# Kernel optimization log

Measured on AMD Instinct MI355X. Metric: run time of the kernel, lower is better.

Reference implementation:

```python
import jax, jax.numpy as jnp
import numpy as np

D_MODEL = 1024
N_HEADS = 16
D_HEAD = D_MODEL // N_HEADS
QLEN = 512
MLEN = 512
BATCH = 8


def setup_inputs() -> dict:
    key = jax.random.key(0)
    ks = jax.random.split(key, 12)
    s = 0.02
    inputs = jax.random.normal(ks[0], (QLEN, BATCH, D_MODEL), jnp.float32)
    r = jax.random.normal(ks[1], (QLEN + MLEN, 1, D_MODEL), jnp.float32)
    u = jax.random.normal(ks[2], (N_HEADS, D_HEAD), jnp.float32) * s
    v = jax.random.normal(ks[3], (N_HEADS, D_HEAD), jnp.float32) * s
    mem = jax.random.normal(ks[4], (MLEN, BATCH, D_MODEL), jnp.float32)
    # attention params (Transformer-XL style): fused qkv, r-projection, output proj
    W_qkv = jax.random.normal(ks[5], (D_MODEL, 3 * D_MODEL), jnp.float32) * s
    W_r = jax.random.normal(ks[6], (D_MODEL, D_MODEL), jnp.float32) * s
    W_o = jax.random.normal(ks[7], (D_MODEL, D_MODEL), jnp.float32) * s
    # GRU params: input-hidden and hidden-hidden for gates (r, z, n), torch layout
    W_ih = jax.random.normal(ks[8], (3 * D_MODEL, D_MODEL), jnp.float32) * s
    W_hh = jax.random.normal(ks[9], (3 * D_MODEL, D_MODEL), jnp.float32) * s
    b_ih = jax.random.normal(ks[10], (3 * D_MODEL,), jnp.float32) * s
    b_hh = jax.random.normal(ks[11], (3 * D_MODEL,), jnp.float32) * s
    h0 = jnp.zeros((BATCH, D_MODEL), jnp.float32)
    return dict(inputs=inputs, r=r, u=u, v=v, mem=mem, W_qkv=W_qkv, W_r=W_r,
                W_o=W_o, W_ih=W_ih, W_hh=W_hh, b_ih=b_ih, b_hh=b_hh, h0=h0)


def _rel_shift(x):
    # x: [q, k, b, h] -> Transformer-XL relative shift
    q, k, b, h = x.shape
    zero_pad = jnp.zeros((q, 1, b, h), x.dtype)
    x_padded = jnp.concatenate([zero_pad, x], axis=1)        # [q, k+1, b, h]
    x_padded = x_padded.reshape(k + 1, q, b, h)
    return x_padded[1:].reshape(q, k, b, h)


def _attention(inputs, r, u, v, mem, W_qkv, W_r, W_o):
    qlen, bsz, _ = inputs.shape
    cat = jnp.concatenate([mem, inputs], axis=0)             # [klen, b, d]
    klen = cat.shape[0]
    qkv = cat @ W_qkv                                        # [klen, b, 3d]
    w_head_q, w_head_k, w_head_v = jnp.split(qkv, 3, axis=-1)
    w_head_q = w_head_q[-qlen:]                              # [q, b, d]
    r_head_k = (r[:, 0, :] @ W_r).reshape(klen, N_HEADS, D_HEAD)  # [k, h, dh]

    q_ = w_head_q.reshape(qlen, bsz, N_HEADS, D_HEAD)
    k_ = w_head_k.reshape(klen, bsz, N_HEADS, D_HEAD)
    v_ = w_head_v.reshape(klen, bsz, N_HEADS, D_HEAD)

    AC = jnp.einsum('ibhd,jbhd->ijbh', q_ + u[None, None], k_)
    BD = jnp.einsum('ibhd,jhd->ijbh', q_ + v[None, None], r_head_k)
    BD = _rel_shift(BD)
    scale = 1.0 / np.sqrt(D_HEAD)
    attn_score = (AC + BD) * scale                           # [q, k, b, h]

    # causal mask with memory: query i attends to keys j <= i + mlen
    mlen = klen - qlen
    i = jnp.arange(qlen)[:, None]
    j = jnp.arange(klen)[None, :]
    mask = j > (i + mlen)                                    # [q, k]
    attn_score = jnp.where(mask[:, :, None, None], -jnp.inf, attn_score)

    attn_prob = jax.nn.softmax(attn_score, axis=1)
    attn_vec = jnp.einsum('ijbh,jbhd->ibhd', attn_prob, v_)
    attn_vec = attn_vec.reshape(qlen, bsz, D_MODEL)
    return attn_vec @ W_o                                    # [q, b, d]


def _gru(x, h0, W_ih, W_hh, b_ih, b_hh):
    # x: [T, B, D]; torch GRU cell math
    Wi_r, Wi_z, Wi_n = jnp.split(W_ih, 3, axis=0)
    Wh_r, Wh_z, Wh_n = jnp.split(W_hh, 3, axis=0)
    bi_r, bi_z, bi_n = jnp.split(b_ih, 3)
    bh_r, bh_z, bh_n = jnp.split(b_hh, 3)

    # precompute input projections for all timesteps
    xr = x @ Wi_r.T + bi_r
    xz = x @ Wi_z.T + bi_z
    xn = x @ Wi_n.T + bi_n

    def step(h, xs):
        xr_t, xz_t, xn_t = xs
        r = jax.nn.sigmoid(xr_t + h @ Wh_r.T + bh_r)
        z = jax.nn.sigmoid(xz_t + h @ Wh_z.T + bh_z)
        n = jnp.tanh(xn_t + r * (h @ Wh_n.T + bh_n))
        h_new = (1.0 - z) * n + z * h
        return h_new, h_new

    _, ys = jax.lax.scan(step, h0, (xr, xz, xn))
    return ys                                                # [T, B, D]


def reference(inputs, r, u, v, mem, W_qkv, W_r, W_o, W_ih, W_hh, b_ih, b_hh, h0):
    y = _attention(inputs, r, u, v, mem, W_qkv, W_r, W_o)
    return _gru(y, h0, W_ih, W_hh, b_ih, b_hh)
```

## Files before the change

### kernel.cpp

```cpp
#include <hip/hip_runtime.h>
#include <math.h>


typedef short bf16x8 __attribute__((ext_vector_type(8)));
typedef float f32x4 __attribute__((ext_vector_type(4)));

union FragU { uint4 u; bf16x8 h; };

#define APAD 65

__device__ inline void split2(float x0, float x1, unsigned& hi, unsigned& lo) {
    unsigned u0 = __float_as_uint(x0), u1 = __float_as_uint(x1);
    float h0 = __uint_as_float(u0 & 0xffff0000u);
    float h1 = __uint_as_float(u1 & 0xffff0000u);
    unsigned l0 = __float_as_uint(x0 - h0), l1 = __float_as_uint(x1 - h1);
    hi = (u0 >> 16) | (u1 & 0xffff0000u);
    lo = (l0 >> 16) | (l1 & 0xffff0000u);
}

__device__ __forceinline__ unsigned long long ld_coh64(const void* p) {
    return __hip_atomic_load((const unsigned long long*)p, __ATOMIC_RELAXED,
                             __HIP_MEMORY_SCOPE_AGENT);
}
__device__ __forceinline__ void st_coh64(void* p, unsigned long long v) {
    __hip_atomic_store((unsigned long long*)p, v, __ATOMIC_RELAXED,
                       __HIP_MEMORY_SCOPE_AGENT);
}

__device__ __forceinline__ void gl_lds16(const uint4* g, uint4* l) {
    __builtin_amdgcn_global_load_lds(
        (const __attribute__((address_space(1))) uint4*)g,
        (__attribute__((address_space(3))) uint4*)l, 16, 0, 0);
}

__device__ __forceinline__ void split_store8(
    const float* x, unsigned* out, int n, int K, int kt, int j)
{
    unsigned h[4], l[4];
    split2(x[0], x[1], h[0], l[0]);
    split2(x[2], x[3], h[1], l[1]);
    split2(x[4], x[5], h[2], l[2]);
    split2(x[6], x[7], h[3], l[3]);
    unsigned* base = out + (size_t)n * K + kt * 32;
    *(uint4*)(base + (((2 * j) ^ (n & 7)) * 4))     = make_uint4(h[0], h[1], h[2], h[3]);
    *(uint4*)(base + (((2 * j + 1) ^ (n & 7)) * 4)) = make_uint4(l[0], l[1], l[2], l[3]);
}

#define SEG0 1048576
#define SEG1 1441792
#define SEG2 1572864
#define SEG3 1703936
#define SEG4 2097152
#define SEG5 2228224

__global__ __launch_bounds__(256) void prep_all(
    const float* __restrict__ mem, const float* __restrict__ inputs,
    const float* __restrict__ Wqkv, const float* __restrict__ Wr,
    const float* __restrict__ Wo, const float* __restrict__ Wih,
    const float* __restrict__ r_in,
    unsigned* __restrict__ catP, unsigned* __restrict__ WqkvP,
    unsigned* __restrict__ WrP, unsigned* __restrict__ WoP,
    unsigned* __restrict__ WihP, unsigned* __restrict__ rP)
{
    int idx = blockIdx.x * 256 + threadIdx.x;
    if (idx >= SEG5) return;
    float x[8];
    if (idx < SEG0) {
        int c = idx & 127, n = idx >> 7;
        int kt = c >> 2, j = c & 3, k = kt * 32 + j * 8;
        const float* src = (n < 4096) ? (mem + (size_t)n * 1024 + k)
                                      : (inputs + (size_t)(n - 4096) * 1024 + k);
        float4 a = *(const float4*)src, b = *(const float4*)(src + 4);
        x[0]=a.x; x[1]=a.y; x[2]=a.z; x[3]=a.w; x[4]=b.x; x[5]=b.y; x[6]=b.z; x[7]=b.w;
        split_store8(x, catP, n, 1024, kt, j);
    } else if (idx < SEG3) {
        int i, Nr, ldw; const float* W; unsigned* out;
        if (idx < SEG1)      { i = idx - SEG0; Nr = 3072; ldw = 3072; W = Wqkv; out = WqkvP; }
        else if (idx < SEG2) { i = idx - SEG1; Nr = 1024; ldw = 1024; W = Wr;   out = WrP;  }
        else                 { i = idx - SEG2; Nr = 1024; ldw = 1024; W = Wo;   out = WoP;  }
        int n = i % Nr, c = i / Nr;
        int kt = c >> 2, j = c & 3, k = kt * 32 + j * 8;
        #pragma unroll
        for (int q = 0; q < 8; ++q) x[q] = W[(size_t)(k + q) * ldw + n];
        split_store8(x, out, n, 1024, kt, j);
    } else {
        int i; const float* W; unsigned* out;
        if (idx < SEG4) { i = idx - SEG3; W = Wih;  out = WihP; }
        else            { i = idx - SEG4; W = r_in; out = rP;   }
        int c = i & 127, n = i >> 7;
        int kt = c >> 2, j = c & 3, k = kt * 32 + j * 8;
        float4 a = *(const float4*)(W + (size_t)n * 1024 + k);
        float4 b = *(const float4*)(W + (size_t)n * 1024 + k + 4);
        x[0]=a.x; x[1]=a.y; x[2]=a.z; x[3]=a.w; x[4]=b.x; x[5]=b.y; x[6]=b.z; x[7]=b.w;
        split_store8(x, out, n, 1024, kt, j);
    }
}

template<bool BIAS, bool SPLITOUT>
__global__ __launch_bounds__(256) void gemm_pp(
    const uint4* __restrict__ Ap4, const uint4* __restrict__ Bp4,
    const float* __restrict__ bias, float* __restrict__ C,
    unsigned* __restrict__ Cp, int K, int ldc)
{
    __shared__ uint4 SH[2048];
    uint4* Ab = SH;
    uint4* Bb = SH + 1024;
    int tid = threadIdx.x;
    int lane = tid & 63, wid = tid >> 6;
    int wr = wid >> 1, wc = wid & 1;
    int n0 = blockIdx.x * 128, m0 = blockIdx.y * 128;
    int r15 = lane & 15, s = lane >> 4;
    int r4 = (lane >> 4) * 4;
    int K4 = K >> 2;

    f32x4 acc[4][4];
    #pragma unroll
    for (int i = 0; i < 4; ++i)
        #pragma unroll
        for (int j = 0; j < 4; ++j) acc[i][j] = 0.0f;

    for (int kt = 0; kt < (K >> 5); ++kt) {
        #pragma unroll
        for (int q = 0; q < 4; ++q) {
            int base = q * 256 + wid * 64;
            int idx  = base + lane;
            int row = idx >> 3, slot = idx & 7;
            gl_lds16(Ap4 + (size_t)(m0 + row) * K4 + kt * 8 + slot, &Ab[base]);
            gl_lds16(Bp4 + (size_t)(n0 + row) * K4 + kt * 8 + slot, &Bb[base]);
        }
        __syncthreads();
        FragU ahi[4], alo[4], bhi[4], blo[4];
        #pragma unroll
        for (int f = 0; f < 4; ++f) {
            int ar = wr * 64 + f * 16 + r15;
            ahi[f].u = Ab[ar * 8 + ((2 * s) ^ (ar & 7))];
            alo[f].u = Ab[ar * 8 + ((2 * s + 1) ^ (ar & 7))];
            int br = wc * 64 + f * 16 + r15;
            bhi[f].u = Bb[br * 8 + ((2 * s) ^ (br & 7))];
            blo[f].u = Bb[br * 8 + ((2 * s + 1) ^ (br & 7))];
        }
        #pragma unroll
        for (int fi = 0; fi < 4; ++fi)
            #pragma unroll
            for (int fj = 0; fj < 4; ++fj) {
                acc[fi][fj] = __builtin_amdgcn_mfma_f32_16x16x32_bf16(ahi[fi].h, bhi[fj].h, acc[fi][fj], 0, 0, 0);
                acc[fi][fj] = __builtin_amdgcn_mfma_f32_16x16x32_bf16(ahi[fi].h, blo[fj].h, acc[fi][fj], 0, 0, 0);
                acc[fi][fj] = __builtin_amdgcn_mfma_f32_16x16x32_bf16(alo[fi].h, bhi[fj].h, acc[fi][fj], 0, 0, 0);
            }
        __syncthreads();
    }

    if (!SPLITOUT) {
        #pragma unroll
        for (int fj = 0; fj < 4; ++fj) {
            int n = n0 + wc * 64 + fj * 16 + r15;
            float bv = BIAS ? bias[n] : 0.f;
            #pragma unroll
            for (int fi = 0; fi < 4; ++fi) {
                int m = m0 + wr * 64 + fi * 16 + r4;
                #pragma unroll
                for (int r = 0; r < 4; ++r)
                    C[(size_t)(m + r) * ldc + n] = acc[fi][fj][r] + bv;
            }
        }
    } else {
        float* Cs = (float*)SH;
        #pragma unroll
        for (int half = 0; half < 2; ++half) {
            __syncthreads();
            if (wr == half) {
                #pragma unroll
                for (int fi = 0; fi < 4; ++fi)
                    #pragma unroll
                    for (int fj = 0; fj < 4; ++fj)
                        #pragma unroll
                        for (int r = 0; r < 4; ++r)
                            Cs[(fi * 16 + r4 + r) * 128 + wc * 64 + fj * 16 + r15] = acc[fi][fj][r];
            }
            __syncthreads();
            #pragma unroll
            for (int q = 0; q < 4; ++q) {
                int oc = q * 256 + tid;
                int lr = oc >> 4, oct = oc & 15;
                float x[8];
                *(float4*)&x[0] = *(float4*)&Cs[lr * 128 + oct * 8];
                *(float4*)&x[4] = *(float4*)&Cs[lr * 128 + oct * 8 + 4];
                int m = m0 + half * 64 + lr;
                int k = n0 + oct * 8;
                split_store8(x, Cp, m, ldc, k >> 5, (k >> 3) & 3);
            }
        }
    }
}

__global__ __launch_bounds__(256) void attn_fused(
    const float* __restrict__ qkv, const float* __restrict__ rk,
    const float* __restrict__ u_, const float* __restrict__ v_,
    unsigned* __restrict__ y1P)
{
    __shared__ float qu[64][APAD], qv[64][APAD], Kt[64][APAD], Vt[64][APAD];
    __shared__ float RKs[128][APAD];
    __shared__ float S[64][APAD];

    int tid = threadIdx.x;
    int it = blockIdx.x, b = blockIdx.y, h = blockIdx.z;
    int i0 = it * 64;
    int ti = tid >> 4, tj = tid & 15;

    {
        int r = tid >> 2, c0 = (tid & 3) * 16;
        size_t base = ((size_t)(i0 + r + 512) * 8 + b) * 3072 + h * 64;
        #pragma unroll
        for (int q = 0; q < 4; ++q) {
            int c = c0 + q * 4;
            float4 qq = *(const float4*)&qkv[base + c];
            float4 uu = *(const float4*)&u_[h * 64 + c];
            float4 vv = *(const float4*)&v_[h * 64 + c];
            *(float4*)&qu[r][c] = make_float4(qq.x + uu.x, qq.y + uu.y, qq.z + uu.z, qq.w + uu.w);
            *(float4*)&qv[r][c] = make_float4(qq.x + vv.x, qq.y + vv.y, qq.z + vv.z, qq.w + vv.w);
        }
    }

    float m[4] = {-1e30f, -1e30f, -1e30f, -1e30f};
    float l[4] = {0.f, 0.f, 0.f, 0.f};
    float Od[4][4] = {};
    int njt = it + 9;

    for (int jt = 0; jt < njt; ++jt) {
        int j0 = jt * 64;
        __syncthreads();
        {
            int r = tid >> 2, c0 = (tid & 3) * 16;
            size_t kb = ((size_t)(j0 + r) * 8 + b) * 3072 + 1024 + h * 64;
            #pragma unroll
            for (int q = 0; q < 4; ++q) {
                int c = c0 + q * 4;
                *(float4*)&Kt[r][c] = *(const float4*)&qkv[kb + c];
                *(float4*)&Vt[r][c] = *(const float4*)&qkv[kb + 1024 + c];
            }
        }
        {
            int r2 = tid >> 1, c0 = (tid & 1) * 32;
            int jj = j0 - i0 + 448 + r2;
            jj = jj < 0 ? 0 : (jj > 1023 ? 1023 : jj);
            size_t rb = (size_t)jj * 1024 + h * 64;
            #pragma unroll
            for (int q = 0; q < 8; ++q) {
                int c = c0 + q * 4;
                *(float4*)&RKs[r2][c] = *(const float4*)&rk[rb + c];
            }
        }
        __syncthreads();

        float acc[4][4] = {};
        int jlb = (tj - ti) * 4 + 60;
        #pragma unroll 4
        for (int d4 = 0; d4 < 64; d4 += 4) {
            float4 Aq[4], Cq[4], Kv[4], Rv[7];
            #pragma unroll
            for (int i = 0; i < 4; ++i) {
                Aq[i] = *(float4*)&qu[ti * 4 + i][d4];
                Cq[i] = *(float4*)&qv[ti * 4 + i][d4];
                Kv[i] = *(float4*)&Kt[tj * 4 + i][d4];
            }
            #pragma unroll
            for (int t = 0; t < 7; ++t)
                Rv[t] = *(float4*)&RKs[jlb + t][d4];
            #pragma unroll
            for (int i = 0; i < 4; ++i)
                #pragma unroll
                for (int j = 0; j < 4; ++j) {
                    float4 kk = Kv[j];
                    float4 rr = Rv[j - i + 3];
                    acc[i][j] += Aq[i].x * kk.x + Aq[i].y * kk.y + Aq[i].z * kk.z + Aq[i].w * kk.w
                               + Cq[i].x * rr.x + Cq[i].y * rr.y + Cq[i].z * rr.z + Cq[i].w * rr.w;
                }
        }
        #pragma unroll
        for (int i = 0; i < 4; ++i) {
            int gi = i0 + ti * 4 + i;
            float mx = -1e30f;
            #pragma unroll
            for (int j = 0; j < 4; ++j) {
                int gj = j0 + tj * 4 + j;
                float vS = acc[i][j] * 0.125f;
                if (gj > gi + 512) vS = -1e30f;
                acc[i][j] = vS;
                mx = fmaxf(mx, vS);
            }
            mx = fmaxf(mx, __shfl_xor(mx, 1));
            mx = fmaxf(mx, __shfl_xor(mx, 2));
            mx = fmaxf(mx, __shfl_xor(mx, 4));
            mx = fmaxf(mx, __shfl_xor(mx, 8));
            float mn = fmaxf(m[i], mx);
            float sc = __expf(m[i] - mn);
            m[i] = mn;
            float4 pv;
            pv.x = __expf(acc[i][0] - mn);
            pv.y = __expf(acc[i][1] - mn);
            pv.z = __expf(acc[i][2] - mn);
            pv.w = __expf(acc[i][3] - mn);
            *(float4*)&S[ti * 4 + i][tj * 4] = pv;
            float ps = pv.x + pv.y + pv.z + pv.w;
            ps += __shfl_xor(ps, 1);
            ps += __shfl_xor(ps, 2);
            ps += __shfl_xor(ps, 4);
            ps += __shfl_xor(ps, 8);
            l[i] = l[i] * sc + ps;
            #pragma unroll
            for (int j2 = 0; j2 < 4; ++j2) Od[i][j2] *= sc;
        }
        asm volatile("" ::: "memory");
        #pragma unroll 4
        for (int jb = 0; jb < 64; jb += 4) {
            float4 p0 = *(float4*)&S[ti * 4 + 0][jb];
            float4 p1 = *(float4*)&S[ti * 4 + 1][jb];
            float4 p2 = *(float4*)&S[ti * 4 + 2][jb];
            float4 p3 = *(float4*)&S[ti * 4 + 3][jb];
            float4 v0 = *(float4*)&Vt[jb + 0][tj * 4];
            float4 v1 = *(float4*)&Vt[jb + 1][tj * 4];
            float4 v2 = *(float4*)&Vt[jb + 2][tj * 4];
            float4 v3 = *(float4*)&Vt[jb + 3][tj * 4];
            float4 pr[4] = {p0, p1, p2, p3};
            #pragma unroll
            for (int i = 0; i < 4; ++i) {
                Od[i][0] += pr[i].x * v0.x + pr[i].y * v1.x + pr[i].z * v2.x + pr[i].w * v3.x;
                Od[i][1] += pr[i].x * v0.y + pr[i].y * v1.y + pr[i].z * v2.y + pr[i].w * v3.y;
                Od[i][2] += pr[i].x * v0.z + pr[i].y * v1.z + pr[i].z * v2.z + pr[i].w * v3.z;
                Od[i][3] += pr[i].x * v0.w + pr[i].y * v1.w + pr[i].z * v2.w + pr[i].w * v3.w;
            }
        }
    }
    #pragma unroll
    for (int i = 0; i < 4; ++i) {
        int ri = ti * 4 + i;
        float inv = 1.f / l[i];
        float4 o = make_float4(Od[i][0] * inv, Od[i][1] * inv, Od[i][2] * inv, Od[i][3] * inv);
        int n = (i0 + ri) * 8 + b;
        unsigned hw0, hw1, lw0, lw1;
        split2(o.x, o.y, hw0, lw0);
        split2(o.z, o.w, hw1, lw1);
        int kt2 = 2 * h + (tj >> 3);
        int j2 = (tj >> 1) & 3;
        int wo = (tj & 1) * 2;
        unsigned* bp = y1P + (size_t)n * 1024 + kt2 * 32;
        *(uint2*)(bp + (((2 * j2)     ^ (n & 7)) * 4) + wo) = make_uint2(hw0, hw1);
        *(uint2*)(bp + (((2 * j2 + 1) ^ (n & 7)) * 4) + wo) = make_uint2(lw0, lw1);
    }
}

__global__ __launch_bounds__(256) void prep_whh(
    const float* __restrict__ Whh, uint4* __restrict__ outp)
{
    int idx = blockIdx.x * 256 + threadIdx.x;
    if (idx >= 393216) return;
    int lane = idx & 63;
    int rest = idx >> 6;
    int gate = rest % 3;
    int kt   = (rest / 3) & 31;
    int g64  = rest / 96;
    int n = gate * 1024 + g64 * 16 + (lane & 15);
    int k = kt * 32 + (lane >> 4) * 8;
    const float* src = Whh + (size_t)n * 1024 + k;
    float4 x0 = *(const float4*)src, x1 = *(const float4*)(src + 4);
    unsigned h[4], l[4];
    split2(x0.x, x0.y, h[0], l[0]);
    split2(x0.z, x0.w, h[1], l[1]);
    split2(x1.x, x1.y, h[2], l[2]);
    split2(x1.z, x1.w, h[3], l[3]);
    outp[((size_t)rest * 2 + 0) * 64 + lane] = make_uint4(h[0], h[1], h[2], h[3]);
    outp[((size_t)rest * 2 + 1) * 64 + lane] = make_uint4(l[0], l[1], l[2], l[3]);
}

__global__ __launch_bounds__(256, 1) void gru_persist2(
    const float* __restrict__ h0, float* __restrict__ hA, float* __restrict__ hB,
    const uint4* __restrict__ WhhG, const float* __restrict__ bhh,
    const float* __restrict__ xg, float* __restrict__ out,
    unsigned* __restrict__ flags)
{
    __shared__ uint4 Bf[4096];
    __shared__ float red[3][64][4];
    int tid = threadIdx.x;
    int lane = tid & 63, wv = tid >> 6;
    int g64 = blockIdx.x;

    int col = lane & 15;
    int d0 = g64 * 16 + (lane >> 4) * 4;
    bool act = (wv == 0) && (col < 8);
    float4 br4 = make_float4(0, 0, 0, 0), bz4 = br4, bn4 = br4;
    if (act) {
        br4 = *(const float4*)&bhh[d0];
        bz4 = *(const float4*)&bhh[1024 + d0];
        bn4 = *(const float4*)&bhh[2048 + d0];
    }
    const uint4* wb = WhhG + (size_t)g64 * 12288 + (wv < 3 ? wv : 0) * 128 + lane;

    for (int t = 0; t < 512; ++t) {
        const float* hi_ = (t == 0) ? h0 : ((t & 1) ? hA : hB);
        float* ho = (t & 1) ? hB : hA;

        float4 xr4, xz4, xn4;
        unsigned long long hp01 = 0, hp23 = 0;
        if (act) {
            size_t xb = ((size_t)t * 8 + col) * 3072 + d0;
            xr4 = *(const float4*)&xg[xb];
            xz4 = *(const float4*)&xg[xb + 1024];
            xn4 = *(const float4*)&xg[xb + 2048];
            hp01 = ld_coh64(hi_ + col * 1024 + d0);
            hp23 = ld_coh64(hi_ + col * 1024 + d0 + 2);
        }

        uint4 wA[16], wB[16];
        #pragma unroll
        for (int q = 0; q < 8; ++q) {
            wA[2 * q]     = wb[q * 384];
            wA[2 * q + 1] = wb[q * 384 + 64];
        }

        unsigned long long hq[16];
        #pragma unroll
        for (int i = 0; i < 4; ++i) {
            int s = i * 256 + tid;
            const float* hp = hi_ + (s & 7) * 1024 + (s >> 5) * 32 + ((s >> 3) & 3) * 8;
            #pragma unroll
            for (int q = 0; q < 4; ++q) hq[i * 4 + q] = ld_coh64(hp + q * 2);
        }
        #pragma unroll
        for (int i = 0; i < 4; ++i) {
            int s = i * 256 + tid;
            int b = s & 7, oct = (s >> 3) & 3, kt = s >> 5;
            float x[8];
            #pragma unroll
            for (int q = 0; q < 4; ++q) {
                x[2 * q]     = __uint_as_float((unsigned)(hq[i * 4 + q] & 0xffffffffu));
                x[2 * q + 1] = __uint_as_float((unsigned)(hq[i * 4 + q] >> 32));
            }
            unsigned hh[4], ll[4];
            split2(x[0], x[1], hh[0], ll[0]);
            split2(x[2], x[3], hh[1], ll[1]);
            split2(x[4], x[5], hh[2], ll[2]);
            split2(x[6], x[7], hh[3], ll[3]);
            int ln = oct * 16 + b;
            Bf[(kt * 2 + 0) * 64 + ln] = make_uint4(hh[0], hh[1], hh[2], hh[3]);
            Bf[(kt * 2 + 1) * 64 + ln] = make_uint4(ll[0], ll[1], ll[2], ll[3]);
        }
        __syncthreads();

        f32x4 acc = 0.0f;
        #define GRU_LOAD(dst, c0)                                   \
            _Pragma("unroll")                                       \
            for (int q = 0; q < 8; ++q) {                           \
                dst[2 * q]     = wb[((c0) * 8 + q) * 384];          \
                dst[2 * q + 1] = wb[((c0) * 8 + q) * 384 + 64];     \
            }
        #define GRU_COMP(src, c0)                                   \
            _Pragma("unroll")                                       \
            for (int q = 0; q < 8; ++q) {                           \
                int kt = (c0) * 8 + q;                              \
                FragU ah, al, bh, bl;                               \
                ah.u = src[2 * q]; al.u = src[2 * q + 1];           \
                bh.u = Bf[(kt * 2 + 0) * 64 + lane];                \
                bl.u = Bf[(kt * 2 + 1) * 64 + lane];                \
                acc = __builtin_amdgcn_mfma_f32_16x16x32_bf16(ah.h, bh.h, acc, 0, 0, 0); \
                acc = __builtin_amdgcn_mfma_f32_16x16x32_bf16(ah.h, bl.h, acc, 0, 0, 0); \
                acc = __builtin_amdgcn_mfma_f32_16x16x32_bf16(al.h, bh.h, acc, 0, 0, 0); \
            }
        if (wv < 3) {
            GRU_LOAD(wB, 1);
            GRU_COMP(wA, 0);
            GRU_LOAD(wA, 2);
            GRU_COMP(wB, 1);
            GRU_LOAD(wB, 3);
            GRU_COMP(wA, 2);
            GRU_COMP(wB, 3);
            *(f32x4*)&red[wv][lane][0] = acc;
        }
        #undef GRU_LOAD
        #undef GRU_COMP
        __syncthreads();

        if (act) {
            f32x4 aR = *(f32x4*)&red[0][lane][0];
            f32x4 aZ = *(f32x4*)&red[1][lane][0];
            f32x4 aN = *(f32x4*)&red[2][lane][0];
            float xr[4] = {xr4.x, xr4.y, xr4.z, xr4.w};
            float xz[4] = {xz4.x, xz4.y, xz4.z, xz4.w};
            float xn[4] = {xn4.x, xn4.y, xn4.z, xn4.w};
            float hp[4] = {__uint_as_float((unsigned)(hp01 & 0xffffffffu)),
                           __uint_as_float((unsigned)(hp01 >> 32)),
                           __uint_as_float((unsigned)(hp23 & 0xffffffffu)),
                           __uint_as_float((unsigned)(hp23 >> 32))};
            float br[4] = {br4.x, br4.y, br4.z, br4.w};
            float bz[4] = {bz4.x, bz4.y, bz4.z, bz4.w};
            float bn[4] = {bn4.x, bn4.y, bn4.z, bn4.w};
            float hn[4];
            #pragma unroll
            for (int r = 0; r < 4; ++r) {
                float rr = 1.f / (1.f + __expf(-(xr[r] + aR[r] + br[r])));
                float zz = 1.f / (1.f + __expf(-(xz[r] + aZ[r] + bz[r])));
                float nn = tanhf(xn[r] + rr * (aN[r] + bn[r]));
                hn[r] = (1.f - zz) * nn + zz * hp[r];
            }
            unsigned long long v01 = (unsigned long long)__float_as_uint(hn[0])
                                   | ((unsigned long long)__float_as_uint(hn[1]) << 32);
            unsigned long long v23 = (unsigned long long)__float_as_uint(hn[2])
                                   | ((unsigned long long)__float_as_uint(hn[3]) << 32);
            st_coh64(ho + col * 1024 + d0, v01);
            st_coh64(ho + col * 1024 + d0 + 2, v23);
            *(float4*)&out[((size_t)t * 8 + col) * 1024 + d0] =
                make_float4(hn[0], hn[1], hn[2], hn[3]);
        }

        if (t != 511) {
            __syncthreads();
            unsigned tgt = (unsigned)t + 1u;
            if (tid < 64) {
                if (tid == 0)
                    __hip_atomic_store(&flags[(size_t)g64 * 16], tgt,
                                       __ATOMIC_RELAXED, __HIP_MEMORY_SCOPE_AGENT);
                const unsigned* fp = &flags[(size_t)tid * 16];
                for (;;) {
                    unsigned f = __hip_atomic_load(fp, __ATOMIC_RELAXED,
                                                   __HIP_MEMORY_SCOPE_AGENT);
                    if (__all(f >= tgt)) break;
                }
            }
            __syncthreads();
        }
    }
}

__global__ __launch_bounds__(192, 1) void gru_step_mfma(
    const float* __restrict__ hin, float* __restrict__ hout,
    const uint4* __restrict__ WhhG, const float* __restrict__ bhh,
    const float* __restrict__ xg, float* __restrict__ out, int t)
{
    __shared__ uint4 Bf[4096];
    __shared__ float red[3][64][4];
    int tid = threadIdx.x;
    int lane = tid & 63, wv = tid >> 6;
    int g64 = blockIdx.x;

    int col = lane & 15;
    int d0 = g64 * 16 + (lane >> 4) * 4;
    bool act = (wv == 0) && (col < 8);
    float4 xr4, xz4, xn4, hp4, br4, bz4, bn4;
    if (act) {
        size_t xb = ((size_t)t * 8 + col) * 3072 + d0;
        xr4 = *(const float4*)&xg[xb];
        xz4 = *(const float4*)&xg[xb + 1024];
        xn4 = *(const float4*)&xg[xb + 2048];
        hp4 = *(const float4*)&hin[col * 1024 + d0];
        br4 = *(const float4*)&bhh[d0];
        bz4 = *(const float4*)&bhh[1024 + d0];
        bn4 = *(const float4*)&bhh[2048 + d0];
    }

    const uint4* wb = WhhG + (size_t)g64 * 12288 + wv * 128 + lane;
    uint4 wA[16], wB[16];
    #pragma unroll
    for (int q = 0; q < 8; ++q) {
        wA[2 * q]     = wb[q * 384];
        wA[2 * q + 1] = wb[q * 384 + 64];
    }

    for (int s = tid; s < 1024; s += 192) {
        int b = s & 7, oct = (s >> 3) & 3, kt = s >> 5;
        const float* hp = hin + b * 1024 + kt * 32 + oct * 8;
        float4 x0 = *(const float4*)hp, x1 = *(const float4*)(hp + 4);
        unsigned hh[4], ll[4];
        split2(x0.x, x0.y, hh[0], ll[0]);
        split2(x0.z, x0.w, hh[1], ll[1]);
        split2(x1.x, x1.y, hh[2], ll[2]);
        split2(x1.z, x1.w, hh[3], ll[3]);
        int ln = oct * 16 + b;
        Bf[(kt * 2 + 0) * 64 + ln] = make_uint4(hh[0], hh[1], hh[2], hh[3]);
        Bf[(kt * 2 + 1) * 64 + ln] = make_uint4(ll[0], ll[1], ll[2], ll[3]);
    }
    __syncthreads();

    f32x4 acc = 0.0f;
    #define GRU_LOAD(dst, c0)                                   \
        _Pragma("unroll")                                       \
        for (int q = 0; q < 8; ++q) {                           \
            dst[2 * q]     = wb[((c0) * 8 + q) * 384];          \
            dst[2 * q + 1] = wb[((c0) * 8 + q) * 384 + 64];     \
        }
    #define GRU_COMP(src, c0)                                   \
        _Pragma("unroll")                                       \
        for (int q = 0; q < 8; ++q) {                           \
            int kt = (c0) * 8 + q;                              \
            FragU ah, al, bh, bl;                               \
            ah.u = src[2 * q]; al.u = src[2 * q + 1];           \
            bh.u = Bf[(kt * 2 + 0) * 64 + lane];                \
            bl.u = Bf[(kt * 2 + 1) * 64 + lane];                \
            acc = __builtin_amdgcn_mfma_f32_16x16x32_bf16(ah.h, bh.h, acc, 0, 0, 0); \
            acc = __builtin_amdgcn_mfma_f32_16x16x32_bf16(ah.h, bl.h, acc, 0, 0, 0); \
            acc = __builtin_amdgcn_mfma_f32_16x16x32_bf16(al.h, bh.h, acc, 0, 0, 0); \
        }
    GRU_LOAD(wB, 1);
    GRU_COMP(wA, 0);
    GRU_LOAD(wA, 2);
    GRU_COMP(wB, 1);
    GRU_LOAD(wB, 3);
    GRU_COMP(wA, 2);
    GRU_COMP(wB, 3);
    #undef GRU_LOAD
    #undef GRU_COMP

    *(f32x4*)&red[wv][lane][0] = acc;
    __syncthreads();

    if (act) {
        f32x4 aR = *(f32x4*)&red[0][lane][0];
        f32x4 aZ = *(f32x4*)&red[1][lane][0];
        f32x4 aN = *(f32x4*)&red[2][lane][0];
        float xr[4] = {xr4.x, xr4.y, xr4.z, xr4.w};
        float xz[4] = {xz4.x, xz4.y, xz4.z, xz4.w};
        float xn[4] = {xn4.x, xn4.y, xn4.z, xn4.w};
        float hp[4] = {hp4.x, hp4.y, hp4.z, hp4.w};
        float br[4] = {br4.x, br4.y, br4.z, br4.w};
        float bz[4] = {bz4.x, bz4.y, bz4.z, bz4.w};
        float bn[4] = {bn4.x, bn4.y, bn4.z, bn4.w};
        float hn[4];
        #pragma unroll
        for (int r = 0; r < 4; ++r) {
            float rr = 1.f / (1.f + __expf(-(xr[r] + aR[r] + br[r])));
            float zz = 1.f / (1.f + __expf(-(xz[r] + aZ[r] + bz[r])));
            float nn = tanhf(xn[r] + rr * (aN[r] + bn[r]));
            hn[r] = (1.f - zz) * nn + zz * hp[r];
        }
        float4 hv = make_float4(hn[0], hn[1], hn[2], hn[3]);
        *(float4*)&hout[col * 1024 + d0] = hv;
        *(float4*)&out[((size_t)t * 8 + col) * 1024 + d0] = hv;
    }
}

extern "C" void kernel_launch(void* const* d_in, const int* in_sizes, int n_in,
                              void* d_out, int out_size, void* d_ws, size_t ws_size,
                              hipStream_t stream) {
    (void)in_sizes; (void)n_in; (void)out_size; (void)ws_size;
    const float* inputs = (const float*)d_in[0];
    const float* r_in   = (const float*)d_in[1];
    const float* u_in   = (const float*)d_in[2];
    const float* v_in   = (const float*)d_in[3];
    const float* mem    = (const float*)d_in[4];
    const float* Wqkv   = (const float*)d_in[5];
    const float* Wr     = (const float*)d_in[6];
    const float* Wo     = (const float*)d_in[7];
    const float* Wih    = (const float*)d_in[8];
    const float* Whh    = (const float*)d_in[9];
    const float* bih    = (const float*)d_in[10];
    const float* bhh    = (const float*)d_in[11];
    const float* h0     = (const float*)d_in[12];
    float* out = (float*)d_out;
    float* ws = (float*)d_ws;

    float*    qkv   = ws;
    float*    rk    = ws + 25165824;
    unsigned* y1P   = (unsigned*)(ws + 26214400);
    unsigned* y2P   = (unsigned*)(ws + 30408704);
    float*    xg    = ws + 34603008;
    float*    hA    = ws + 47185920;
    float*    hB    = ws + 47194112;
    unsigned* WqkvP = (unsigned*)(ws + 47202304);
    unsigned* WrP   = (unsigned*)(ws + 50348032);
    unsigned* WoP   = (unsigned*)(ws + 51396608);
    unsigned* WihP  = (unsigned*)(ws + 52445184);
    unsigned* flags = (unsigned*)(ws + 55590912);
    uint4*    WhhG  = (uint4*)qkv;
    unsigned* catP  = (unsigned*)xg;
    unsigned* rP    = (unsigned*)xg + 8388608;

    dim3 blk(256);
    hipMemsetAsync(flags, 0, 4096, stream);
    prep_all<<<8704, blk, 0, stream>>>(mem, inputs, Wqkv, Wr, Wo, Wih, r_in,
                                       catP, WqkvP, WrP, WoP, WihP, rP);

    gemm_pp<false, false><<<dim3(16, 32), blk, 0, stream>>>(
        (const uint4*)catP, (const uint4*)WqkvP + 1024 * 256, nullptr,
        qkv + 1024, nullptr, 1024, 3072);
    gemm_pp<false, false><<<dim3(24, 32), blk, 0, stream>>>(
        (const uint4*)catP + 4096 * 256, (const uint4*)WqkvP, nullptr,
        qkv + (size_t)4096 * 3072, nullptr, 1024, 3072);
    gemm_pp<false, false><<<dim3(8, 8), blk, 0, stream>>>(
        (const uint4*)rP, (const uint4*)WrP, nullptr, rk, nullptr, 1024, 1024);
    attn_fused<<<dim3(8, 8, 16), blk, 0, stream>>>(qkv, rk, u_in, v_in, y1P);
    prep_whh<<<1536, blk, 0, stream>>>(Whh, WhhG);
    gemm_pp<false, true><<<dim3(8, 32), blk, 0, stream>>>(
        (const uint4*)y1P, (const uint4*)WoP, nullptr, nullptr, y2P, 1024, 1024);
    gemm_pp<true, false><<<dim3(24, 32), blk, 0, stream>>>(
        (const uint4*)y2P, (const uint4*)WihP, bih, xg, nullptr, 1024, 3072);

    {
        const float* a0 = h0; float* a1 = hA; float* a2 = hB;
        const uint4* a3 = WhhG; const float* a4 = bhh; const float* a5 = xg;
        float* a6 = out; unsigned* a7 = flags;
        void* args[8] = {&a0, &a1, &a2, &a3, &a4, &a5, &a6, &a7};
        hipError_t e = hipLaunchCooperativeKernel((void*)gru_persist2,
                                                  dim3(64), dim3(256), args, 0, stream);
        if (e != hipSuccess) {
            const float* hin = h0;
            for (int s = 0; s < 512; ++s) {
                float* hp = (s & 1) ? hB : hA;
                gru_step_mfma<<<64, dim3(192), 0, stream>>>(hin, hp, WhhG, bhh, xg, out, s);
                hin = hp;
            }
        }
    }
}
```

Baseline: 4.735 ms.

## Overlap GRU input-projection GEMM with persistent recurrence in one cooperative kernel

Removes the separate xg GEMM launch and folds it into the cooperative GRU kernel. Extra blocks (64 beyond the 64 recurrence blocks) compute 128x128 tiles of the input projection and publish per-row-block completion counters. The recurrence blocks spin on those counters every 16 timesteps before reading xg with coherent loads. This overlaps the input-projection GEMM with the serial recurrence, at the cost of scalar atomic stores and spin-waiting. It also changes APAD from 65 to 68.

```diff
diff --git a/kernel.cpp b/kernel.cpp
--- a/kernel.cpp
+++ b/kernel.cpp
@@ -7,7 +7,9 @@
 
 union FragU { uint4 u; bf16x8 h; };
 
-#define APAD 65
+#define APAD 68
+#define ULO(v) __uint_as_float((unsigned)((v) & 0xffffffffu))
+#define UHI(v) __uint_as_float((unsigned)((v) >> 32))
 
 __device__ inline void split2(float x0, float x1, unsigned& hi, unsigned& lo) {
     unsigned u0 = __float_as_uint(x0), u1 = __float_as_uint(x1);
@@ -25,6 +27,9 @@
 __device__ __forceinline__ void st_coh64(void* p, unsigned long long v) {
     __hip_atomic_store((unsigned long long*)p, v, __ATOMIC_RELAXED,
                        __HIP_MEMORY_SCOPE_AGENT);
+}
+__device__ __forceinline__ void st_coh32(float* p, float v) {
+    __hip_atomic_store(p, v, __ATOMIC_RELAXED, __HIP_MEMORY_SCOPE_AGENT);
 }
 
 __device__ __forceinline__ void gl_lds16(const uint4* g, uint4* l) {
@@ -372,15 +377,84 @@
     outp[((size_t)rest * 2 + 1) * 64 + lane] = make_uint4(l[0], l[1], l[2], l[3]);
 }
 
-__global__ __launch_bounds__(256, 1) void gru_persist2(
+__global__ __launch_bounds__(256, 1) void gru_xg_fused(
     const float* __restrict__ h0, float* __restrict__ hA, float* __restrict__ hB,
     const uint4* __restrict__ WhhG, const float* __restrict__ bhh,
-    const float* __restrict__ xg, float* __restrict__ out,
-    unsigned* __restrict__ flags)
+    float* __restrict__ xg,
+    const uint4* __restrict__ y2P, const uint4* __restrict__ WihP,
+    const float* __restrict__ bih,
+    float* __restrict__ out, unsigned* __restrict__ flags,
+    unsigned* __restrict__ xgcnt)
 {
-    __shared__ uint4 Bf[4096];
-    __shared__ float red[3][64][4];
+    __shared__ uint4 SMEM[4288];
     int tid = threadIdx.x;
+
+    if (blockIdx.x >= 64) {
+        uint4* Ab = SMEM;
+        uint4* Bb = SMEM + 1024;
+        int lane = tid & 63, wid = tid >> 6;
+        int wr = wid >> 1, wc = wid & 1;
+        int r15 = lane & 15, s = lane >> 4;
+        int r4q = (lane >> 4) * 4;
+        for (int T = (int)blockIdx.x - 64; T < 768; T += 64) {
+            int m0 = (T / 24) * 128, n0 = (T % 24) * 128;
+            f32x4 acc[4][4];
+            #pragma unroll
+            for (int i = 0; i < 4; ++i)
+                #pragma unroll
+                for (int j = 0; j < 4; ++j) acc[i][j] = 0.0f;
+            for (int kt = 0; kt < 32; ++kt) {
+                #pragma unroll
+                for (int q = 0; q < 4; ++q) {
+                    int base = q * 256 + wid * 64;
+                    int idx  = base + lane;
+                    int row = idx >> 3, slot = idx & 7;
+                    gl_lds16(y2P + (size_t)(m0 + row) * 256 + kt * 8 + slot, &Ab[base]);
+                    gl_lds16(WihP + (size_t)(n0 + row) * 256 + kt * 8 + slot, &Bb[base]);
+                }
+                __syncthreads();
+                FragU ahi[4], alo[4], bhi[4], blo[4];
+                #pragma unroll
+                for (int f = 0; f < 4; ++f) {
+                    int ar = wr * 64 + f * 16 + r15;
+                    ahi[f].u = Ab[ar * 8 + ((2 * s) ^ (ar & 7))];
+                    alo[f].u = Ab[ar * 8 + ((2 * s + 1) ^ (ar & 7))];
+                    int br = wc * 64 + f * 16 + r15;
+                    bhi[f].u = Bb[br * 8 + ((2 * s) ^ (br & 7))];
+                    blo[f].u = Bb[br * 8 + ((2 * s + 1) ^ (br & 7))];
+                }
+                #pragma unroll
+                for (int fi = 0; fi < 4; ++fi)
+                    #pragma unroll
+                    for (int fj = 0; fj < 4; ++fj) {
+                        acc[fi][fj] = __builtin_amdgcn_mfma_f32_16x16x32_bf16(ahi[fi].h, bhi[fj].h, acc[fi][fj], 0, 0, 0);
+                        acc[fi][fj] = __builtin_amdgcn_mfma_f32_16x16x32_bf16(ahi[fi].h, blo[fj].h, acc[fi][fj], 0, 0, 0);
+                        acc[fi][fj] = __builtin_amdgcn_mfma_f32_16x16x32_bf16(alo[fi].h, bhi[fj].h, acc[fi][fj], 0, 0, 0);
+                    }
+                __syncthreads();
+            }
+            #pragma unroll
+            for (int fj = 0; fj < 4; ++fj) {
+                int n = n0 + wc * 64 + fj * 16 + r15;
+                float bv = bih[n];
+                #pragma unroll
+                for (int fi = 0; fi < 4; ++fi) {
+                    int mr = m0 + wr * 64 + fi * 16 + r4q;
+                    #pragma unroll
+                    for (int r = 0; r < 4; ++r)
+                        st_coh32(&xg[(size_t)(mr + r) * 3072 + n], acc[fi][fj][r] + bv);
+                }
+            }
+            __syncthreads();
+            if (tid == 0)
+                __hip_atomic_fetch_add(&xgcnt[(size_t)(T / 24) * 16], 1u,
+                                       __ATOMIC_RELAXED, __HIP_MEMORY_SCOPE_AGENT);
+        }
+        return;
+    }
+
+    uint4* Bf = SMEM;
+    float* red = (float*)(SMEM + 4096);
     int lane = tid & 63, wv = tid >> 6;
     int g64 = blockIdx.x;
 
@@ -399,13 +473,18 @@
         const float* hi_ = (t == 0) ? h0 : ((t & 1) ? hA : hB);
         float* ho = (t & 1) ? hB : hA;
 
-        float4 xr4, xz4, xn4;
+        unsigned long long xr01 = 0, xr23 = 0, xz01 = 0, xz23 = 0, xn01 = 0, xn23 = 0;
         unsigned long long hp01 = 0, hp23 = 0;
         if (act) {
+            if ((t & 15) == 0) {
+                const unsigned* xf = xgcnt + (size_t)(t >> 4) * 16;
+                while (__hip_atomic_load(xf, __ATOMIC_RELAXED,
+                                         __HIP_MEMORY_SCOPE_AGENT) < 24u) {}
+            }
             size_t xb = ((size_t)t * 8 + col) * 3072 + d0;
-            xr4 = *(const float4*)&xg[xb];
-            xz4 = *(const float4*)&xg[xb + 1024];
-            xn4 = *(const float4*)&xg[xb + 2048];
+            xr01 = ld_coh64(&xg[xb]);        xr23 = ld_coh64(&xg[xb + 2]);
+            xz01 = ld_coh64(&xg[xb + 1024]); xz23 = ld_coh64(&xg[xb + 1026]);
+            xn01 = ld_coh64(&xg[xb + 2048]); xn23 = ld_coh64(&xg[xb + 2050]);
             hp01 = ld_coh64(hi_ + col * 1024 + d0);
             hp23 = ld_coh64(hi_ + col * 1024 + d0 + 2);
         }
@@ -432,8 +511,8 @@
             float x[8];
             #pragma unroll
             for (int q = 0; q < 4; ++q) {
-                x[2 * q]     = __uint_as_float((unsigned)(hq[i * 4 + q] & 0xffffffffu));
-                x[2 * q + 1] = __uint_as_float((unsigned)(hq[i * 4 + q] >> 32));
+                x[2 * q]     = ULO(hq[i * 4 + q]);
+                x[2 * q + 1] = UHI(hq[i * 4 + q]);
             }
             unsigned hh[4], ll[4];
             split2(x[0], x[1], hh[0], ll[0]);
@@ -473,23 +552,20 @@
             GRU_LOAD(wB, 3);
             GRU_COMP(wA, 2);
             GRU_COMP(wB, 3);
-            *(f32x4*)&red[wv][lane][0] = acc;
+            *(f32x4*)&red[(wv * 64 + lane) * 4] = acc;
         }
         #undef GRU_LOAD
         #undef GRU_COMP
         __syncthreads();
 
         if (act) {
-            f32x4 aR = *(f32x4*)&red[0][lane][0];
-            f32x4 aZ = *(f32x4*)&red[1][lane][0];
-            f32x4 aN = *(f32x4*)&red[2][lane][0];
-            float xr[4] = {xr4.x, xr4.y, xr4.z, xr4.w};
-            float xz[4] = {xz4.x, xz4.y, xz4.z, xz4.w};
-            float xn[4] = {xn4.x, xn4.y, xn4.z, xn4.w};
-            float hp[4] = {__uint_as_float((unsigned)(hp01 & 0xffffffffu)),
-                           __uint_as_float((unsigned)(hp01 >> 32)),
-                           __uint_as_float((unsigned)(hp23 & 0xffffffffu)),
-                           __uint_as_float((unsigned)(hp23 >> 32))};
+            f32x4 aR = *(f32x4*)&red[(0 * 64 + lane) * 4];
+            f32x4 aZ = *(f32x4*)&red[(1 * 64 + lane) * 4];
+            f32x4 aN = *(f32x4*)&red[(2 * 64 + lane) * 4];
+            float xr[4] = {ULO(xr01), UHI(xr01), ULO(xr23), UHI(xr23)};
+            float xz[4] = {ULO(xz01), UHI(xz01), ULO(xz23), UHI(xz23)};
+            float xn[4] = {ULO(xn01), UHI(xn01), ULO(xn23), UHI(xn23)};
+            float hp[4] = {ULO(hp01), UHI(hp01), ULO(hp23), UHI(hp23)};
             float br[4] = {br4.x, br4.y, br4.z, br4.w};
             float bz[4] = {bz4.x, bz4.y, bz4.z, bz4.w};
             float bn[4] = {bn4.x, bn4.y, bn4.z, bn4.w};
@@ -668,12 +744,13 @@
     unsigned* WoP   = (unsigned*)(ws + 51396608);
     unsigned* WihP  = (unsigned*)(ws + 52445184);
     unsigned* flags = (unsigned*)(ws + 55590912);
+    unsigned* xgcnt = (unsigned*)(ws + 55590912) + 1024;
     uint4*    WhhG  = (uint4*)qkv;
     unsigned* catP  = (unsigned*)xg;
     unsigned* rP    = (unsigned*)xg + 8388608;
 
     dim3 blk(256);
-    hipMemsetAsync(flags, 0, 4096, stream);
+    (void)hipMemsetAsync(flags, 0, 6144, stream);
     prep_all<<<8704, blk, 0, stream>>>(mem, inputs, Wqkv, Wr, Wo, Wih, r_in,
                                        catP, WqkvP, WrP, WoP, WihP, rP);
 
@@ -689,17 +766,19 @@
     prep_whh<<<1536, blk, 0, stream>>>(Whh, WhhG);
     gemm_pp<false, true><<<dim3(8, 32), blk, 0, stream>>>(
         (const uint4*)y1P, (const uint4*)WoP, nullptr, nullptr, y2P, 1024, 1024);
-    gemm_pp<true, false><<<dim3(24, 32), blk, 0, stream>>>(
-        (const uint4*)y2P, (const uint4*)WihP, bih, xg, nullptr, 1024, 3072);
 
     {
         const float* a0 = h0; float* a1 = hA; float* a2 = hB;
-        const uint4* a3 = WhhG; const float* a4 = bhh; const float* a5 = xg;
-        float* a6 = out; unsigned* a7 = flags;
-        void* args[8] = {&a0, &a1, &a2, &a3, &a4, &a5, &a6, &a7};
-        hipError_t e = hipLaunchCooperativeKernel((void*)gru_persist2,
-                                                  dim3(64), dim3(256), args, 0, stream);
+        const uint4* a3 = WhhG; const float* a4 = bhh; float* a5 = xg;
+        const uint4* a6 = (const uint4*)y2P; const uint4* a7 = (const uint4*)WihP;
+        const float* a8 = bih; float* a9 = out;
+        unsigned* a10 = flags; unsigned* a11 = xgcnt;
+        void* args[12] = {&a0, &a1, &a2, &a3, &a4, &a5, &a6, &a7, &a8, &a9, &a10, &a11};
+        hipError_t e = hipLaunchCooperativeKernel((void*)gru_xg_fused,
+                                                  dim3(128), dim3(256), args, 0, stream);
         if (e != hipSuccess) {
+            gemm_pp<true, false><<<dim3(24, 32), blk, 0, stream>>>(
+                (const uint4*)y2P, (const uint4*)WihP, bih, xg, nullptr, 1024, 3072);
             const float* hin = h0;
             for (int s = 0; s < 512; ++s) {
                 float* hp = (s & 1) ? hB : hA;
```

After: 4.731 ms. No clear change (-0.1%).
